# Optimization experiments

Hardware: AMD Instinct MI355X
Metric: run time of the kernel (lower is better)

The kernel has to match this reference:

```python
import jax, jax.numpy as jnp
import numpy as np

B, L, HID = 4, 2048, 2048
H, D = 16, 128
BASE = 10000.0
NEG = -1e30


def _rope_tables(seq_len, dim, dtype):
    # inv_freq: (dim/2,), emb = concat(freqs, freqs): (L, dim)
    inv_freq = 1.0 / (BASE ** (jnp.arange(0, dim, 2, dtype=jnp.float32) / dim))
    t = jnp.arange(seq_len, dtype=jnp.float32)
    freqs = t[:, None] * inv_freq[None, :]          # (L, dim/2)
    emb = jnp.concatenate([freqs, freqs], axis=-1)  # (L, dim)
    return jnp.cos(emb).astype(dtype), jnp.sin(emb).astype(dtype)


def _rotate_half(x):
    x1, x2 = x[..., : x.shape[-1] // 2], x[..., x.shape[-1] // 2 :]
    return jnp.concatenate([-x2, x1], axis=-1)


def setup_inputs() -> dict:
    key = jax.random.key(0)
    k1, k2, k3 = jax.random.split(key, 3)
    x = jax.random.normal(k1, (B, L, HID), dtype=jnp.float32)
    # qkv init std = sqrt(2/(5*hidden)); fc xavier std ~ sqrt(2/(in+out))
    Wqkv = jax.random.normal(k2, (HID, 3 * H * D), dtype=jnp.float32) * np.sqrt(2.0 / (5.0 * HID))
    Wo = jax.random.normal(k3, (H * D, HID), dtype=jnp.float32) * np.sqrt(2.0 / (H * D + HID))
    return {"x": x, "Wqkv": Wqkv, "Wo": Wo}


def reference(x, Wqkv, Wo):
    b, l, _ = x.shape
    qkv = (x @ Wqkv).reshape(b, l, 3, H, D).transpose(2, 0, 3, 1, 4)  # (3,b,h,l,d)
    q, k, v = qkv[0], qkv[1], qkv[2]
    cos, sin = _rope_tables(l, D, x.dtype)  # (l, D) each, broadcasts over (b,h,l,d)
    q = q * cos + _rotate_half(q) * sin
    k = k * cos + _rotate_half(k) * sin
    scale = 1.0 / np.sqrt(D)
    scores = jnp.einsum("bhqd,bhkd->bhqk", q, k) * scale  # (b,h,l,l)
    causal = jnp.tril(jnp.ones((l, l), dtype=bool))
    scores = jnp.where(causal, scores, NEG)
    att = jax.nn.softmax(scores, axis=-1)
    out = jnp.einsum("bhqk,bhkd->bhqd", att, v)  # (b,h,l,d)
    out = out.transpose(0, 2, 1, 3).reshape(b, l, H * D)
    return out @ Wo
```

## Files before the change

### kernel.cpp

```cpp
#include <hip/hip_runtime.h>
#include <hip/hip_bf16.h>
#include <stdint.h>

typedef unsigned short ushort_t;
typedef __bf16 bf16x8 __attribute__((ext_vector_type(8)));
typedef float    f32x4 __attribute__((ext_vector_type(4)));
typedef float   f32x16 __attribute__((ext_vector_type(16)));
typedef unsigned short us4 __attribute__((ext_vector_type(4)));
typedef unsigned int ui4 __attribute__((ext_vector_type(4)));

#define QK_SCALE 0.12751744f
#define NEG_BIG  -1e30f

__device__ __forceinline__ unsigned short f2bf(float f) {
    union { float f; unsigned int u; } v; v.f = f;
    unsigned int u = v.u;
    return (unsigned short)((u + 0x7FFFu + ((u >> 16) & 1u)) >> 16);
}

__device__ __forceinline__ unsigned int pk2bf(float a, float b) {
    unsigned int r;
    asm("v_cvt_pk_bf16_f32 %0, %1, %2" : "=v"(r) : "v"(a), "v"(b));
    return r;
}

__device__ __forceinline__ void gload16(const void* g, void* l) {
    __builtin_amdgcn_global_load_lds(
        (__attribute__((address_space(1))) void*)(uintptr_t)g,
        (__attribute__((address_space(3))) void*)(uint32_t)(uintptr_t)l,
        16, 0, 0);
}


__global__ __launch_bounds__(256) void cvt_bf16_kernel(
    const float4* __restrict__ in, us4* __restrict__ out, int n4) {
    int i = blockIdx.x * 256 + threadIdx.x;
    if (i >= n4) return;
    float4 v = in[i];
    us4 o; o[0] = f2bf(v.x); o[1] = f2bf(v.y); o[2] = f2bf(v.z); o[3] = f2bf(v.w);
    out[i] = o;
}

__global__ __launch_bounds__(256) void transpose_bf16(
    const float* __restrict__ in, ushort_t* __restrict__ out, int R, int C) {
    __shared__ float t[64][65];
    int c0 = blockIdx.x * 64, r0 = blockIdx.y * 64;
    int cc = threadIdx.x & 63, rr = threadIdx.x >> 6;
#pragma unroll
    for (int i = 0; i < 16; ++i) {
        int r = i * 4 + rr;
        t[r][cc] = in[(size_t)(r0 + r) * C + c0 + cc];
    }
    __syncthreads();
#pragma unroll
    for (int i = 0; i < 16; ++i) {
        int r = i * 4 + rr;
        out[(size_t)(c0 + r) * R + r0 + cc] = f2bf(t[cc][r]);
    }
}

__global__ __launch_bounds__(256) void rope_table_kernel(float2* __restrict__ rope) {
    int i = blockIdx.x * 256 + threadIdx.x;
    int l = i >> 6, j = i & 63;
    float inv = exp2f((float)j * -0.20762050593046f);
    float f = (float)l * inv;
    rope[i] = make_float2(cosf(f), sinf(f));
}


template <int EPI>
__global__ __launch_bounds__(256, 2)
void gemm_bt(const ushort_t* __restrict__ A, const ushort_t* __restrict__ Bt,
             int M, int N, int K,
             float* __restrict__ C,
             ushort_t* __restrict__ Qb, ushort_t* __restrict__ Kb,
             ushort_t* __restrict__ Vt, const float2* __restrict__ rope) {
    constexpr int MI = (EPI == 1) ? 2 : 4;
    constexpr int NI = (EPI == 1) ? 8 : 4;

    __shared__ __attribute__((aligned(16))) ushort_t ldsA[128 * 64];
    __shared__ __attribute__((aligned(16))) ushort_t ldsB[128 * 64];
    char* ldsAc = (char*)ldsA;
    char* ldsBc = (char*)ldsB;

    const int tid  = threadIdx.x;
    const int lane = tid & 63, wid = tid >> 6;
    const int lr = lane & 15, lg = lane >> 4;

    const int nbn = N >> 7;
    const int nwg = gridDim.x;
    const int bid = blockIdx.x;
    const int wg  = (bid & 7) * (nwg >> 3) + (bid >> 3);
    const int bm  = wg / nbn, bn = wg % nbn;

    const int arow0 = (EPI == 1) ? wid * 32 : (wid >> 1) * 64;
    const int bcol0 = (EPI == 1) ? 0        : (wid & 1) * 64;

    const int colb = ((tid & 7) << 4) ^ (((tid >> 3) & 7) << 4);
    const int rowi = tid >> 3;
    const char* Ap = (const char*)A + ((size_t)(bm * 128 + rowi) * K) * 2 + colb;
    const char* Bp = (const char*)Bt + ((size_t)(bn * 128 + rowi) * K) * 2 + colb;
    const size_t rstr = (size_t)32 * K * 2;
    char* ldA = ldsAc + wid * 1024;
    char* ldB = ldsBc + wid * 1024;

    f32x4 acc[MI][NI];
#pragma unroll
    for (int i = 0; i < MI; ++i)
#pragma unroll
        for (int j = 0; j < NI; ++j) acc[i][j] = (f32x4){0.f, 0.f, 0.f, 0.f};

    for (int k0 = 0; k0 < K; k0 += 64) {
#pragma unroll
        for (int r = 0; r < 4; ++r) {
            gload16(Ap + r * rstr + (size_t)k0 * 2, ldA + r * 4096);
            gload16(Bp + r * rstr + (size_t)k0 * 2, ldB + r * 4096);
        }
        __syncthreads();
#pragma unroll
        for (int kk = 0; kk < 2; ++kk) {
            bf16x8 af[MI], bfv[NI];
#pragma unroll
            for (int mi = 0; mi < MI; ++mi) {
                int row = arow0 + mi * 16 + lr;
                int off = (row << 7) + kk * 64 + lg * 16;
                off ^= (row & 7) << 4;
                af[mi] = *(const bf16x8*)(ldsAc + off);
            }
#pragma unroll
            for (int ni = 0; ni < NI; ++ni) {
                int row = bcol0 + ni * 16 + lr;
                int off = (row << 7) + kk * 64 + lg * 16;
                off ^= (row & 7) << 4;
                bfv[ni] = *(const bf16x8*)(ldsBc + off);
            }
#pragma unroll
            for (int mi = 0; mi < MI; ++mi)
#pragma unroll
                for (int ni = 0; ni < NI; ++ni)
                    acc[mi][ni] = __builtin_amdgcn_mfma_f32_16x16x32_bf16(
                        af[mi], bfv[ni], acc[mi][ni], 0, 0, 0);
        }
        __syncthreads();
    }

    if constexpr (EPI == 0) {
#pragma unroll
        for (int mi = 0; mi < MI; ++mi) {
            int gr0 = bm * 128 + arow0 + mi * 16 + lg * 4;
#pragma unroll
            for (int ni = 0; ni < NI; ++ni) {
                int gc = bn * 128 + bcol0 + ni * 16 + lr;
#pragma unroll
                for (int r = 0; r < 4; ++r)
                    C[(size_t)(gr0 + r) * N + gc] = acc[mi][ni][r];
            }
        }
    } else {
        const int which = bn >> 4, h = bn & 15;
#pragma unroll
        for (int mi = 0; mi < MI; ++mi) {
            int gr0 = bm * 128 + arow0 + mi * 16 + lg * 4;
            int b = gr0 >> 11, l0 = gr0 & 2047;
            if (which == 2) {
#pragma unroll
                for (int ni = 0; ni < NI; ++ni) {
                    int d = ni * 16 + lr;
                    us4 pk;
#pragma unroll
                    for (int r = 0; r < 4; ++r) pk[r] = f2bf(acc[mi][ni][r]);
                    *(us4*)(Vt + ((size_t)(b * 16 + h) * 128 + d) * 2048 + l0) = pk;
                }
            } else {
                ushort_t* dst = (which == 0) ? Qb : Kb;
                const float sc = (which == 0) ? QK_SCALE : 1.0f;
#pragma unroll
                for (int ni = 0; ni < 4; ++ni) {
                    int j = ni * 16 + lr;
#pragma unroll
                    for (int r = 0; r < 4; ++r) {
                        float2 cs = rope[(size_t)(l0 + r) * 64 + j];
                        float x1 = acc[mi][ni][r], x2 = acc[mi][ni + 4][r];
                        size_t base = ((size_t)(b * 16 + h) * 2048 + (l0 + r)) * 128;
                        dst[base + j]      = f2bf((x1 * cs.x - x2 * cs.y) * sc);
                        dst[base + j + 64] = f2bf((x2 * cs.x + x1 * cs.y) * sc);
                    }
                }
            }
        }
    }
}


__global__ __attribute__((amdgpu_flat_work_group_size(512, 512), amdgpu_waves_per_eu(2, 2)))
void attn_fwd(const ushort_t* __restrict__ Qb, const ushort_t* __restrict__ Kb,
              const ushort_t* __restrict__ Vt, ushort_t* __restrict__ AO) {
    constexpr int L = 2048;
    __shared__ __attribute__((aligned(16))) char smem[65536];

    const int tid  = threadIdx.x;
    const int lane = tid & 63, wid = tid >> 6;
    const int q_l  = lane & 31;
    const int hi   = lane >> 5;

    const int bid  = blockIdx.x;
    const int hl   = (bid >> 3) & 7;
    const int pr   = bid >> 6;
    const int head = (bid & 7) * 8 + hl;

    const ushort_t* Qh = Qb + (size_t)head * L * 128;
    const char*     KhB = (const char*)(Kb + (size_t)head * L * 128);
    const char*     VhB = (const char*)(Vt + (size_t)head * 128 * L);
    const int b = head >> 4, h = head & 15;

    int rK[2], cK[2], rV[2], cV[2];
#pragma unroll
    for (int i = 0; i < 2; ++i) {
        rK[i] = wid * 8 + i * 4 + (lane >> 4);
        cK[i] = ((lane & 15) << 4) ^ ((rK[i] & 7) << 4);
        rV[i] = wid * 16 + i * 8 + (lane >> 3);
        cV[i] = ((lane & 7) << 4) ^ ((rV[i] & 7) << 4);
    }
    const int kdst = wid * 2048;
    const int vdst = 16384 + wid * 2048;

    for (int ph = 0; ph < 2; ++ph) {
        const int s     = ph ? (7 - pr) : pr;
        const int q0w   = s * 256 + wid * 32;
        const int ntile = 4 * s + 4;

        bf16x8 qf[8];
#pragma unroll
        for (int sb = 0; sb < 8; ++sb)
            qf[sb] = *(const bf16x8*)(Qh + (size_t)(q0w + q_l) * 128 + sb * 16 + hi * 8);

        f32x16 o[4];
#pragma unroll
        for (int d0 = 0; d0 < 4; ++d0) o[d0] = (f32x16)(0.f);
        float m_ = -__builtin_inff(), l_ = 0.f;

        __syncthreads();
#pragma unroll
        for (int i = 0; i < 2; ++i) {
            gload16(KhB + (size_t)(rK[i]) * 256 + cK[i],              smem + kdst + i * 1024);
            gload16(VhB + (size_t)rV[i] * 4096 + cV[i],               smem + vdst + i * 1024);
        }

        for (int t = 0; t < ntile; ++t) {
            __syncthreads();
            const int kb = (t & 1) * 32768;
            const int nb = ((t + 1) & 1) * 32768;
            if (t + 1 < ntile) {
                const int kn = 64 * (t + 1);
#pragma unroll
                for (int i = 0; i < 2; ++i) {
                    gload16(KhB + (size_t)(kn + rK[i]) * 256 + cK[i], smem + nb + kdst + i * 1024);
                    gload16(VhB + (size_t)rV[i] * 4096 + (size_t)kn * 2 + cV[i], smem + nb + vdst + i * 1024);
                }
            }

            const int k0 = 64 * t;
            if (k0 > q0w + 31) continue;

            const bool do1 = (k0 + 32 <= q0w + 31);

            f32x16 s0, s1;
            {
                bf16x8 kf[8];
#pragma unroll
                for (int sb = 0; sb < 8; ++sb) {
                    int off = kb + q_l * 256 + ((sb * 32 + hi * 16) ^ ((q_l & 7) << 4));
                    kf[sb] = *(const bf16x8*)(smem + off);
                }
                f32x16 sA = (f32x16)(0.f), sB = (f32x16)(0.f);
#pragma unroll
                for (int sb = 0; sb < 8; sb += 2) {
                    sA = __builtin_amdgcn_mfma_f32_32x32x16_bf16(kf[sb],     qf[sb],     sA, 0, 0, 0);
                    sB = __builtin_amdgcn_mfma_f32_32x32x16_bf16(kf[sb + 1], qf[sb + 1], sB, 0, 0, 0);
                }
                s0 = sA + sB;
            }
            if (do1) {
                bf16x8 kf[8];
#pragma unroll
                for (int sb = 0; sb < 8; ++sb) {
                    int off = kb + (32 + q_l) * 256 + ((sb * 32 + hi * 16) ^ ((q_l & 7) << 4));
                    kf[sb] = *(const bf16x8*)(smem + off);
                }
                f32x16 sA = (f32x16)(0.f), sB = (f32x16)(0.f);
#pragma unroll
                for (int sb = 0; sb < 8; sb += 2) {
                    sA = __builtin_amdgcn_mfma_f32_32x32x16_bf16(kf[sb],     qf[sb],     sA, 0, 0, 0);
                    sB = __builtin_amdgcn_mfma_f32_32x32x16_bf16(kf[sb + 1], qf[sb + 1], sB, 0, 0, 0);
                }
                s1 = sA + sB;
            }

            if (k0 + 31 > q0w) {
#pragma unroll
                for (int r = 0; r < 16; ++r) {
                    int crow = (r & 3) + 8 * (r >> 2) + 4 * hi;
                    if (k0 + crow > q0w + q_l) s0[r] = NEG_BIG;
                }
            }
            if (do1 && (k0 + 63 > q0w)) {
#pragma unroll
                for (int r = 0; r < 16; ++r) {
                    int crow = (r & 3) + 8 * (r >> 2) + 4 * hi;
                    if (k0 + 32 + crow > q0w + q_l) s1[r] = NEG_BIG;
                }
            }

            float t8[8];
#pragma unroll
            for (int r = 0; r < 8; ++r) t8[r] = fmaxf(s0[r], s0[r + 8]);
            if (do1)
#pragma unroll
                for (int r = 0; r < 8; ++r) t8[r] = fmaxf(t8[r], fmaxf(s1[r], s1[r + 8]));
#pragma unroll
            for (int r = 0; r < 4; ++r) t8[r] = fmaxf(t8[r], t8[r + 4]);
            float tmax = fmaxf(fmaxf(t8[0], t8[1]), fmaxf(t8[2], t8[3]));
            tmax = fmaxf(tmax, __shfl_xor(tmax, 32, 64));

            if (!__all(tmax <= m_ + 8.f)) {
                float mn = fmaxf(m_, tmax);
                float alpha = exp2f(m_ - mn);
                m_ = mn;
                l_ *= alpha;
#pragma unroll
                for (int d0 = 0; d0 < 4; ++d0)
#pragma unroll
                    for (int r = 0; r < 16; ++r) o[d0][r] *= alpha;
            }

            float rs = 0.f;
#pragma unroll
            for (int r = 0; r < 16; ++r) { s0[r] = exp2f(s0[r] - m_); rs += s0[r]; }
            if (do1)
#pragma unroll
                for (int r = 0; r < 16; ++r) { s1[r] = exp2f(s1[r] - m_); rs += s1[r]; }
            rs += __shfl_xor(rs, 32, 64);
            l_ += rs;

            bf16x8 pfA[2], pfB[2];
            {
                unsigned int pk[8], po[8];
#pragma unroll
                for (int i = 0; i < 8; ++i) pk[i] = pk2bf(s0[2 * i], s0[2 * i + 1]);
#pragma unroll
                for (int i = 0; i < 8; ++i) po[i] = __shfl_xor(pk[i], 32, 64);
#pragma unroll
                for (int ks = 0; ks < 2; ++ks) {
                    ui4 dw;
                    dw[0] = hi ? po[ks * 4 + 2] : pk[ks * 4 + 0];
                    dw[1] = hi ? po[ks * 4 + 3] : pk[ks * 4 + 1];
                    dw[2] = hi ? pk[ks * 4 + 2] : po[ks * 4 + 0];
                    dw[3] = hi ? pk[ks * 4 + 3] : po[ks * 4 + 1];
                    pfA[ks] = __builtin_bit_cast(bf16x8, dw);
                }
            }
            if (do1) {
                unsigned int pk[8], po[8];
#pragma unroll
                for (int i = 0; i < 8; ++i) pk[i] = pk2bf(s1[2 * i], s1[2 * i + 1]);
#pragma unroll
                for (int i = 0; i < 8; ++i) po[i] = __shfl_xor(pk[i], 32, 64);
#pragma unroll
                for (int ks = 0; ks < 2; ++ks) {
                    ui4 dw;
                    dw[0] = hi ? po[ks * 4 + 2] : pk[ks * 4 + 0];
                    dw[1] = hi ? po[ks * 4 + 3] : pk[ks * 4 + 1];
                    dw[2] = hi ? pk[ks * 4 + 2] : po[ks * 4 + 0];
                    dw[3] = hi ? pk[ks * 4 + 3] : po[ks * 4 + 1];
                    pfB[ks] = __builtin_bit_cast(bf16x8, dw);
                }
            }

            const int vb = kb + 16384;
#pragma unroll
            for (int d0 = 0; d0 < 4; ++d0) {
                int d = d0 * 32 + q_l;
#pragma unroll
                for (int ks = 0; ks < 2; ++ks) {
                    int off = vb + d * 128 + ((ks * 32 + hi * 16) ^ ((d & 7) << 4));
                    bf16x8 vf = *(const bf16x8*)(smem + off);
                    o[d0] = __builtin_amdgcn_mfma_f32_32x32x16_bf16(vf, pfA[ks], o[d0], 0, 0, 0);
                }
                if (do1) {
#pragma unroll
                    for (int ks = 0; ks < 2; ++ks) {
                        int off = vb + d * 128 + (((2 + ks) * 32 + hi * 16) ^ ((d & 7) << 4));
                        bf16x8 vf = *(const bf16x8*)(smem + off);
                        o[d0] = __builtin_amdgcn_mfma_f32_32x32x16_bf16(vf, pfB[ks], o[d0], 0, 0, 0);
                    }
                }
            }
        }

        const float inv = 1.f / l_;
        const size_t rowbase = ((size_t)(b * 2048 + q0w + q_l)) * 2048 + h * 128;
#pragma unroll
        for (int d0 = 0; d0 < 4; ++d0)
#pragma unroll
            for (int g = 0; g < 4; ++g) {
                us4 v;
#pragma unroll
                for (int r = 0; r < 4; ++r) v[r] = f2bf(o[d0][g * 4 + r] * inv);
                *(us4*)(AO + rowbase + d0 * 32 + g * 8 + hi * 4) = v;
            }
    }
}


extern "C" void kernel_launch(void* const* d_in, const int* in_sizes, int n_in,
                              void* d_out, int out_size, void* d_ws, size_t ws_size,
                              hipStream_t stream) {
    const float* x    = (const float*)d_in[0];
    const float* Wqkv = (const float*)d_in[1];
    const float* Wo   = (const float*)d_in[2];
    float* out = (float*)d_out;

    char* w = (char*)d_ws;
    ushort_t* xb   = (ushort_t*)(w);
    ushort_t* W1t  = (ushort_t*)(w + 33554432);
    ushort_t* Wot  = (ushort_t*)(w + 58720256);
    ushort_t* Qb   = (ushort_t*)(w + 67108864);
    ushort_t* Kbf  = (ushort_t*)(w + 100663296);
    ushort_t* Vt   = (ushort_t*)(w + 134217728);
    ushort_t* AO   = (ushort_t*)(w + 167772160);
    float2*   rope = (float2*)(w + 201326592);

    cvt_bf16_kernel<<<16384, 256, 0, stream>>>((const float4*)x, (us4*)xb, 4194304);
    transpose_bf16<<<dim3(96, 32), 256, 0, stream>>>(Wqkv, W1t, 2048, 6144);
    transpose_bf16<<<dim3(32, 32), 256, 0, stream>>>(Wo, Wot, 2048, 2048);
    rope_table_kernel<<<512, 256, 0, stream>>>(rope);

    gemm_bt<1><<<3072, 256, 0, stream>>>(xb, W1t, 8192, 6144, 2048,
                                         nullptr, Qb, Kbf, Vt, rope);
    attn_fwd<<<256, 512, 0, stream>>>(Qb, Kbf, Vt, AO);
    gemm_bt<0><<<1024, 256, 0, stream>>>(AO, Wot, 8192, 2048, 2048,
                                         out, nullptr, nullptr, nullptr, nullptr);
}
```

Baseline: 479.6 us.

## Replace GEMMs with 256x256 double-buffered pipelined kernel and permute Wqkv columns for RoPE

Both projection GEMMs move from 128x128 single-buffered tiles to 256x256 tiles with 512 threads. The 128 KB of LDS is split into two buffers, loads for the next K slices are staged in fine-grained steps interleaved with MFMA quadrants, and progress is tracked with explicit vmcnt waits and barriers. Wqkv columns for Q and K are permuted during the weight transpose, so each wave's tile holds matching RoPE pairs and the rotary epilogue can run inside a 64-column wave tile. This targets global-load latency and the barrier stalls of the old loop, and reuses each tile across more output. The cost is higher register and LDS use and a much smaller grid (256 blocks for the output GEMM), which may underfill the 256 CUs.

Measured after the change: 418.9 us. 1.14x faster.

```diff
diff --git a/kernel.cpp b/kernel.cpp
--- a/kernel.cpp
+++ b/kernel.cpp
@@ -11,6 +11,10 @@
 
 #define QK_SCALE 0.12751744f
 #define NEG_BIG  -1e30f
+
+#define BARRIER() do { asm volatile("" ::: "memory"); __builtin_amdgcn_s_barrier(); asm volatile("" ::: "memory"); } while (0)
+#define VMCNT(N)  asm volatile("s_waitcnt vmcnt(" #N ")" ::: "memory")
+#define MFMA16(d, a, b) d = __builtin_amdgcn_mfma_f32_16x16x32_bf16(a, b, d, 0, 0, 0)
 
 __device__ __forceinline__ unsigned short f2bf(float f) {
     union { float f; unsigned int u; } v; v.f = f;
@@ -59,6 +63,32 @@
     }
 }
 
+__global__ __launch_bounds__(256) void transpose_wqkv(
+    const float* __restrict__ in , ushort_t* __restrict__ out ) {
+    __shared__ float t[64][65];
+    int c0 = blockIdx.x * 64, r0 = blockIdx.y * 64;
+    int cc = threadIdx.x & 63, rr = threadIdx.x >> 6;
+    int n = c0 + cc;
+    int which = n >> 11;
+    int src = n;
+    if (which < 2) {
+        int h = (n >> 7) & 15, p = n & 127;
+        int po = (p & 15) | (((p >> 5) & 3) << 4) | (((p >> 4) & 1) << 6);
+        src = (which << 11) + (h << 7) + po;
+    }
+#pragma unroll
+    for (int i = 0; i < 16; ++i) {
+        int r = i * 4 + rr;
+        t[r][cc] = in[(size_t)(r0 + r) * 6144 + src];
+    }
+    __syncthreads();
+#pragma unroll
+    for (int i = 0; i < 16; ++i) {
+        int r = i * 4 + rr;
+        out[(size_t)(c0 + r) * 2048 + r0 + cc] = f2bf(t[cc][r]);
+    }
+}
+
 __global__ __launch_bounds__(256) void rope_table_kernel(float2* __restrict__ rope) {
     int i = blockIdx.x * 256 + threadIdx.x;
     int l = i >> 6, j = i & 63;
@@ -69,121 +99,162 @@
 
 
 template <int EPI>
-__global__ __launch_bounds__(256, 2)
-void gemm_bt(const ushort_t* __restrict__ A, const ushort_t* __restrict__ Bt,
+__global__ __launch_bounds__(512, 2)
+void gemm256(const ushort_t* __restrict__ A, const ushort_t* __restrict__ Bt,
              int M, int N, int K,
              float* __restrict__ C,
              ushort_t* __restrict__ Qb, ushort_t* __restrict__ Kb,
              ushort_t* __restrict__ Vt, const float2* __restrict__ rope) {
-    constexpr int MI = (EPI == 1) ? 2 : 4;
-    constexpr int NI = (EPI == 1) ? 8 : 4;
-
-    __shared__ __attribute__((aligned(16))) ushort_t ldsA[128 * 64];
-    __shared__ __attribute__((aligned(16))) ushort_t ldsB[128 * 64];
-    char* ldsAc = (char*)ldsA;
-    char* ldsBc = (char*)ldsB;
+    __shared__ __attribute__((aligned(16))) char lds[131072];
 
     const int tid  = threadIdx.x;
     const int lane = tid & 63, wid = tid >> 6;
     const int lr = lane & 15, lg = lane >> 4;
-
-    const int nbn = N >> 7;
+    const int wr = wid >> 2, wc = wid & 3;
+
+    const int nbn = N >> 8;
     const int nwg = gridDim.x;
     const int bid = blockIdx.x;
     const int wg  = (bid & 7) * (nwg >> 3) + (bid >> 3);
     const int bm  = wg / nbn, bn = wg % nbn;
 
-    const int arow0 = (EPI == 1) ? wid * 32 : (wid >> 1) * 64;
-    const int bcol0 = (EPI == 1) ? 0        : (wid & 1) * 64;
-
-    const int colb = ((tid & 7) << 4) ^ (((tid >> 3) & 7) << 4);
-    const int rowi = tid >> 3;
-    const char* Ap = (const char*)A + ((size_t)(bm * 128 + rowi) * K) * 2 + colb;
-    const char* Bp = (const char*)Bt + ((size_t)(bn * 128 + rowi) * K) * 2 + colb;
-    const size_t rstr = (size_t)32 * K * 2;
-    char* ldA = ldsAc + wid * 1024;
-    char* ldB = ldsBc + wid * 1024;
-
-    f32x4 acc[MI][NI];
-#pragma unroll
-    for (int i = 0; i < MI; ++i)
-#pragma unroll
-        for (int j = 0; j < NI; ++j) acc[i][j] = (f32x4){0.f, 0.f, 0.f, 0.f};
-
-    for (int k0 = 0; k0 < K; k0 += 64) {
-#pragma unroll
-        for (int r = 0; r < 4; ++r) {
-            gload16(Ap + r * rstr + (size_t)k0 * 2, ldA + r * 4096);
-            gload16(Bp + r * rstr + (size_t)k0 * 2, ldB + r * 4096);
-        }
-        __syncthreads();
-#pragma unroll
-        for (int kk = 0; kk < 2; ++kk) {
-            bf16x8 af[MI], bfv[NI];
-#pragma unroll
-            for (int mi = 0; mi < MI; ++mi) {
-                int row = arow0 + mi * 16 + lr;
-                int off = (row << 7) + kk * 64 + lg * 16;
-                off ^= (row & 7) << 4;
-                af[mi] = *(const bf16x8*)(ldsAc + off);
-            }
-#pragma unroll
-            for (int ni = 0; ni < NI; ++ni) {
-                int row = bcol0 + ni * 16 + lr;
-                int off = (row << 7) + kk * 64 + lg * 16;
-                off ^= (row & 7) << 4;
-                bfv[ni] = *(const bf16x8*)(ldsBc + off);
-            }
-#pragma unroll
-            for (int mi = 0; mi < MI; ++mi)
-#pragma unroll
-                for (int ni = 0; ni < NI; ++ni)
-                    acc[mi][ni] = __builtin_amdgcn_mfma_f32_16x16x32_bf16(
-                        af[mi], bfv[ni], acc[mi][ni], 0, 0, 0);
-        }
-        __syncthreads();
-    }
+    const int srow = tid >> 3;
+    const int scol = ((tid & 7) << 4) ^ ((srow & 7) << 4);
+    const size_t rowK2 = (size_t)K * 2;
+    const char* sA0 = (const char*)A + ((size_t)(bm * 256 + srow)) * rowK2 + scol;
+    const char* sA1 = sA0 + 128 * rowK2;
+    const char* sB0 = (const char*)Bt + ((size_t)(bn * 256 + srow)) * rowK2 + scol;
+    const char* sB1 = sB0 + 128 * rowK2;
+
+    auto stg = [&](const char* s, int ch, int kt, int dst) {
+        gload16(s + (size_t)(ch * 64) * rowK2 + (size_t)kt * 128, lds + dst + wid * 1024);
+    };
+
+    const int xk0 = (lg * 16) ^ ((lr & 7) << 4);
+    const int xk1 = (64 + lg * 16) ^ ((lr & 7) << 4);
+    const int rowA = wr * 16384 + lr * 128;
+    const int rowB = 32768 + (wc >> 1) * 16384 + ((wc & 1) * 64 + lr) * 128;
+
+    auto rdA = [&](int bu, int mi, int kk) -> bf16x8 {
+        return *(const bf16x8*)(lds + bu * 65536 + rowA + mi * 2048 + (kk ? xk1 : xk0));
+    };
+    auto rdB = [&](int bu, int ni, int kk) -> bf16x8 {
+        return *(const bf16x8*)(lds + bu * 65536 + rowB + ni * 2048 + (kk ? xk1 : xk0));
+    };
+
+    f32x4 acc[8][4];
+#pragma unroll
+    for (int m = 0; m < 8; ++m)
+#pragma unroll
+        for (int n = 0; n < 4; ++n) acc[m][n] = (f32x4){0.f, 0.f, 0.f, 0.f};
+
+    bf16x8 aF[4][2], bF[2][2];
+
+#define RD_A(BU, MH) do { _Pragma("unroll") for (int mi = 0; mi < 4; ++mi) { \
+        aF[mi][0] = rdA(BU, (MH)*4 + mi, 0); aF[mi][1] = rdA(BU, (MH)*4 + mi, 1); } } while (0)
+#define RD_B(BU, NH) do { _Pragma("unroll") for (int ni = 0; ni < 2; ++ni) { \
+        bF[ni][0] = rdB(BU, (NH)*2 + ni, 0); bF[ni][1] = rdB(BU, (NH)*2 + ni, 1); } } while (0)
+#define QUAD(MH, NH) do { __builtin_amdgcn_s_setprio(1); \
+        _Pragma("unroll") for (int kk = 0; kk < 2; ++kk) \
+        _Pragma("unroll") for (int mi = 0; mi < 4; ++mi) \
+        _Pragma("unroll") for (int ni = 0; ni < 2; ++ni) \
+            MFMA16(acc[(MH)*4 + mi][(NH)*2 + ni], aF[mi][kk], bF[ni][kk]); \
+        __builtin_amdgcn_s_setprio(0); } while (0)
+
+    stg(sA0, 0, 0, 0);     stg(sA0, 1, 0, 8192);
+    stg(sA1, 0, 0, 16384); stg(sA1, 1, 0, 24576);
+    stg(sB0, 0, 0, 32768); stg(sB0, 1, 0, 40960);
+    stg(sB1, 0, 0, 49152); stg(sB1, 1, 0, 57344);
+    stg(sA0, 1, 1, 73728); stg(sA1, 1, 1, 90112);
+    stg(sB0, 0, 1, 98304); stg(sB0, 1, 1, 106496);
+    VMCNT(4);
+    BARRIER();
+
+    const int NIT = K / 128;
+    for (int i = 0; i < NIT; ++i) {
+        const int to = 2 * i + 1, te2 = 2 * i + 2, to2 = 2 * i + 3;
+        const bool g = (i + 1 < NIT);
+
+        RD_A(0, 0); RD_B(0, 0);
+        stg(sB1, 0, to, 114688); stg(sB1, 1, to, 122880);
+        BARRIER(); QUAD(0, 0); BARRIER();
+
+        RD_A(0, 1);
+        stg(sA0, 0, to, 65536); stg(sA1, 0, to, 81920);
+        BARRIER(); QUAD(1, 0); BARRIER();
+
+        RD_B(0, 1);
+        if (g) { stg(sA0, 1, te2, 8192); stg(sA1, 1, te2, 24576); }
+        BARRIER(); QUAD(1, 1); BARRIER();
+
+        RD_A(0, 0);
+        if (g) { stg(sB0, 0, te2, 32768); stg(sB0, 1, te2, 40960); VMCNT(4); }
+        else   { VMCNT(0); }
+        BARRIER(); QUAD(0, 1); BARRIER();
+
+        RD_A(1, 0); RD_B(1, 0);
+        if (g) { stg(sB1, 0, te2, 49152); stg(sB1, 1, te2, 57344); }
+        BARRIER(); QUAD(0, 0); BARRIER();
+
+        RD_A(1, 1);
+        if (g) { stg(sA0, 0, te2, 0); stg(sA1, 0, te2, 16384); }
+        BARRIER(); QUAD(1, 0); BARRIER();
+
+        RD_B(1, 1);
+        if (g) { stg(sA0, 1, to2, 73728); stg(sA1, 1, to2, 90112); }
+        BARRIER(); QUAD(1, 1); BARRIER();
+
+        RD_A(1, 0);
+        if (g) { stg(sB0, 0, to2, 98304); stg(sB0, 1, to2, 106496); VMCNT(4); }
+        BARRIER(); QUAD(0, 1); BARRIER();
+    }
+
+#undef RD_A
+#undef RD_B
+#undef QUAD
 
     if constexpr (EPI == 0) {
 #pragma unroll
-        for (int mi = 0; mi < MI; ++mi) {
-            int gr0 = bm * 128 + arow0 + mi * 16 + lg * 4;
-#pragma unroll
-            for (int ni = 0; ni < NI; ++ni) {
-                int gc = bn * 128 + bcol0 + ni * 16 + lr;
+        for (int m = 0; m < 8; ++m) {
+            int gr0 = bm * 256 + wr * 128 + m * 16 + lg * 4;
+#pragma unroll
+            for (int n = 0; n < 4; ++n) {
+                int gc = bn * 256 + wc * 64 + n * 16 + lr;
 #pragma unroll
                 for (int r = 0; r < 4; ++r)
-                    C[(size_t)(gr0 + r) * N + gc] = acc[mi][ni][r];
+                    C[(size_t)(gr0 + r) * N + gc] = acc[m][n][r];
             }
         }
     } else {
-        const int which = bn >> 4, h = bn & 15;
-#pragma unroll
-        for (int mi = 0; mi < MI; ++mi) {
-            int gr0 = bm * 128 + arow0 + mi * 16 + lg * 4;
+        const int hc = bn * 2 + (wc >> 1);
+        const int which = hc >> 4, h = hc & 15;
+#pragma unroll
+        for (int m = 0; m < 8; ++m) {
+            int gr0 = bm * 256 + wr * 128 + m * 16 + lg * 4;
             int b = gr0 >> 11, l0 = gr0 & 2047;
             if (which == 2) {
 #pragma unroll
-                for (int ni = 0; ni < NI; ++ni) {
-                    int d = ni * 16 + lr;
+                for (int n = 0; n < 4; ++n) {
+                    int d = (wc & 1) * 64 + n * 16 + lr;
                     us4 pk;
 #pragma unroll
-                    for (int r = 0; r < 4; ++r) pk[r] = f2bf(acc[mi][ni][r]);
+                    for (int r = 0; r < 4; ++r) pk[r] = f2bf(acc[m][n][r]);
                     *(us4*)(Vt + ((size_t)(b * 16 + h) * 128 + d) * 2048 + l0) = pk;
                 }
             } else {
                 ushort_t* dst = (which == 0) ? Qb : Kb;
                 const float sc = (which == 0) ? QK_SCALE : 1.0f;
 #pragma unroll
-                for (int ni = 0; ni < 4; ++ni) {
-                    int j = ni * 16 + lr;
+                for (int np = 0; np < 4; np += 2) {
+                    int tbl = ((wc & 1) * 2 + (np >> 1)) * 16 + lr;
+                    int p1 = (wc & 1) * 64 + np * 16 + lr;
 #pragma unroll
                     for (int r = 0; r < 4; ++r) {
-                        float2 cs = rope[(size_t)(l0 + r) * 64 + j];
-                        float x1 = acc[mi][ni][r], x2 = acc[mi][ni + 4][r];
+                        float2 cs = rope[(size_t)(l0 + r) * 64 + tbl];
+                        float x1 = acc[m][np][r], x2 = acc[m][np + 1][r];
                         size_t base = ((size_t)(b * 16 + h) * 2048 + (l0 + r)) * 128;
-                        dst[base + j]      = f2bf((x1 * cs.x - x2 * cs.y) * sc);
-                        dst[base + j + 64] = f2bf((x2 * cs.x + x1 * cs.y) * sc);
+                        dst[base + p1]      = f2bf((x1 * cs.x - x2 * cs.y) * sc);
+                        dst[base + p1 + 16] = f2bf((x2 * cs.x + x1 * cs.y) * sc);
                     }
                 }
             }
@@ -431,13 +502,13 @@
     float2*   rope = (float2*)(w + 201326592);
 
     cvt_bf16_kernel<<<16384, 256, 0, stream>>>((const float4*)x, (us4*)xb, 4194304);
-    transpose_bf16<<<dim3(96, 32), 256, 0, stream>>>(Wqkv, W1t, 2048, 6144);
+    transpose_wqkv<<<dim3(96, 32), 256, 0, stream>>>(Wqkv, W1t);
     transpose_bf16<<<dim3(32, 32), 256, 0, stream>>>(Wo, Wot, 2048, 2048);
     rope_table_kernel<<<512, 256, 0, stream>>>(rope);
 
-    gemm_bt<1><<<3072, 256, 0, stream>>>(xb, W1t, 8192, 6144, 2048,
-                                         nullptr, Qb, Kbf, Vt, rope);
+    gemm256<1><<<768, 512, 0, stream>>>(xb, W1t, 8192, 6144, 2048,
+                                        nullptr, Qb, Kbf, Vt, rope);
     attn_fwd<<<256, 512, 0, stream>>>(Qb, Kbf, Vt, AO);
-    gemm_bt<0><<<1024, 256, 0, stream>>>(AO, Wot, 8192, 2048, 2048,
-                                         out, nullptr, nullptr, nullptr, nullptr);
-}
+    gemm256<0><<<256, 512, 0, stream>>>(AO, Wot, 8192, 2048, 2048,
+                                        out, nullptr, nullptr, nullptr, nullptr);
+}
```
